# Optimization experiments

Measured on AMD Instinct MI355X. Metric: run time of the kernel, lower is better.

The kernel has to match this reference:

```python
import jax, jax.numpy as jnp
import numpy as np

N = 64       # number of sites / qubits
CHI = 32     # bond dimension chi_max
D = 2        # physical dim (== label dim l)
BATCH = 262144
STD = 0.001  # init noise, matches MPS.initialize_params


def setup_inputs() -> dict:
    key = jax.random.key(0)
    kx, k0, kc, kn = jax.random.split(key, 4)
    # X: [N, batch, d] -- each X[i] contracts with site i's physical leg
    X = jax.random.normal(kx, (N, BATCH, D), dtype=jnp.float32)
    # core0: (d, chi), one-hot column 0 plus noise
    core0 = jnp.zeros((D, CHI), jnp.float32).at[:, 0].set(1.0)
    core0 = core0 + STD * jax.random.normal(k0, (D, CHI), dtype=jnp.float32)
    # middle cores: (N-1, chi, d, chi), identity stacked over d plus noise
    eye = jnp.eye(CHI, dtype=jnp.float32)                      # (chi, chi)
    mid = jnp.broadcast_to(eye[:, None, :], (CHI, D, CHI))     # (chi, d, chi)
    cores = jnp.broadcast_to(mid, (N - 1, CHI, D, CHI))
    cores = cores + STD * jax.random.normal(kc, (N - 1, CHI, D, CHI), dtype=jnp.float32)
    # coreN: (chi, d), one-hot row 0 plus noise
    coreN = jnp.zeros((CHI, D), jnp.float32).at[0].set(1.0)
    coreN = coreN + STD * jax.random.normal(kn, (CHI, D), dtype=jnp.float32)
    return {"X": X, "core0": core0, "cores": cores, "coreN": coreN}


def reference(X, core0, cores, coreN):
    # Sequential MPS chain contraction:
    #   v <- X[0] @ core0                       (batch, chi)
    #   v <- einsum('ab,bqc,aq->ac', v, core_i, X[i])   for i = 1..N-1
    #   out = |v @ coreN|                       (batch, l)
    v0 = jnp.einsum('aq,qc->ac', X[0], core0)  # (B, chi)

    def step(v, inp):
        x, core = inp  # x: (B, d), core: (chi, d, chi)
        # contract bond then physical leg, keeping only (B, chi) resident
        v_new = jnp.einsum('ab,bqc,aq->ac', v, core, x)
        return v_new, None

    v, _ = jax.lax.scan(step, v0, (X[1:], cores))
    out = jnp.einsum('ac,cq->aq', v, coreN)    # (B, l)
    return jnp.abs(out)
```

## Files before the change

### kernel.cpp

```cpp
#include <hip/hip_runtime.h>
#include <hip/hip_bf16.h>

#define BATCH 262144
#define NSITES 64
#define NJ 2
#define BLOCK_BATCH (64 * NJ)

typedef __attribute__((ext_vector_type(8))) short short8;
typedef __attribute__((ext_vector_type(4))) float f32x4;

__device__ __forceinline__ unsigned cvt_pk_bf16(float a, float b) {
  unsigned r;
  asm("v_cvt_pk_bf16_f32 %0, %1, %2" : "=v"(r) : "v"(a), "v"(b));
  return r;
}

__device__ __forceinline__ int qmap(int k) {
  return (((k >> 2) & 1) << 4) | (((k >> 3) & 3) << 2) | (k & 3);
}

__global__ void pack_E(const float* __restrict__ cores, unsigned short* __restrict__ Ep) {
  int idx = blockIdx.x * 256 + threadIdx.x;
  if (idx >= (NSITES - 1) * 2048) return;
  int t = idx & 7;
  int l = (idx >> 3) & 63;
  int f = (idx >> 9) & 3;
  int p = idx >> 11;
  int g = l >> 4, col = l & 15;
  int m = f >> 1, h = f & 1;
  int k = 8 * g + t, c = h * 16 + col;
  int b = qmap(k);
  float val = cores[((p * 32 + b) * 2 + m) * 32 + c] - ((b == c) ? 1.0f : 0.0f);
  __hip_bfloat16 hv = __float2bfloat16(val);
  Ep[idx] = *(unsigned short*)&hv;
}

__device__ __forceinline__ void gll16(const void* g, void* l) {
  __builtin_amdgcn_global_load_lds(
      (const __attribute__((address_space(1))) unsigned*)g,
      (__attribute__((address_space(3))) unsigned*)l, 16, 0, 0);
}

#define BODYJ(jj, xx0, xx1)                                                     \
  {                                                                             \
    union { short8 s8; unsigned u[4]; } vb;                                     \
    vb.u[0] = cvt_pk_bf16(v[jj][0], v[jj][1]);                                  \
    vb.u[1] = cvt_pk_bf16(v[jj][2], v[jj][3]);                                  \
    vb.u[2] = cvt_pk_bf16(v[jj][4], v[jj][5]);                                  \
    vb.u[3] = cvt_pk_bf16(v[jj][6], v[jj][7]);                                  \
    const f32x4 z = {0.f, 0.f, 0.f, 0.f};                                       \
    f32x4 r0lo = __builtin_amdgcn_mfma_f32_16x16x32_bf16(A0, vb.s8, z, 0, 0, 0); \
    f32x4 r0hi = __builtin_amdgcn_mfma_f32_16x16x32_bf16(A1, vb.s8, z, 0, 0, 0); \
    f32x4 r1lo = __builtin_amdgcn_mfma_f32_16x16x32_bf16(A2, vb.s8, z, 0, 0, 0); \
    f32x4 r1hi = __builtin_amdgcn_mfma_f32_16x16x32_bf16(A3, vb.s8, z, 0, 0, 0); \
    const float ss = (xx0) + (xx1);                                             \
    _Pragma("unroll") for (int t = 0; t < 4; ++t) {                             \
      v[jj][t] = ss * v[jj][t] + (xx0)*r0lo[t] + (xx1)*r1lo[t];                 \
      v[jj][4 + t] = ss * v[jj][4 + t] + (xx0)*r0hi[t] + (xx1)*r1hi[t];         \
    }                                                                           \
  }

__global__ __launch_bounds__(256, 8) void mps_chain_kernel(
    const float* __restrict__ X, const float* __restrict__ core0,
    const float* __restrict__ coreN, const unsigned short* __restrict__ Ep,
    float* __restrict__ out) {
  __shared__ __align__(16) char Elds[2][4096];
  const int tid = threadIdx.x;
  const int lane = tid & 63;
  const int wave = tid >> 6;
  const int col = lane & 15;
  const int g = lane >> 4;
  const int abase = blockIdx.x * BLOCK_BATCH + wave * (16 * NJ);
  const char* Epc = (const char*)Ep;

  gll16(Epc + (size_t)tid * 16, &Elds[0][wave * 1024]);

  float c0[2][8];
#pragma unroll
  for (int m = 0; m < 2; ++m)
#pragma unroll
    for (int t = 0; t < 8; ++t) c0[m][t] = core0[m * 32 + qmap(8 * g + t)];

  float v[NJ][8];
#pragma unroll
  for (int jj = 0; jj < NJ; ++jj) {
    const float2 xj = *(const float2*)(X + 2 * (size_t)(abase + jj * 16 + col));
#pragma unroll
    for (int t = 0; t < 8; ++t) v[jj][t] = xj.x * c0[0][t] + xj.y * c0[1][t];
  }

  float xl[NJ], xh[NJ];
#pragma unroll
  for (int jj = 0; jj < NJ; ++jj) {
    const float2 t_ =
        *(const float2*)(X + 2 * ((size_t)1 * BATCH + abase + jj * 16 + col));
    xl[jj] = t_.x;
    xh[jj] = t_.y;
  }
  __syncthreads();

#pragma unroll 1
  for (int s = 1; s < NSITES; ++s) {
    const int buf = (s - 1) & 1;
    if (s < NSITES - 1)
      gll16(Epc + (size_t)s * 4096 + (size_t)tid * 16, &Elds[buf ^ 1][wave * 1024]);

    const size_t sx = (s + 1 < NSITES) ? (size_t)(s + 1) : (size_t)(NSITES - 1);
    float2 xn[NJ];
#pragma unroll
    for (int jj = 0; jj < NJ; ++jj)
      xn[jj] = *(const float2*)(X + 2 * (sx * BATCH + abase + jj * 16 + col));

    const short8* ep = (const short8*)&Elds[buf][lane * 16];
    const short8 A0 = ep[0], A1 = ep[64], A2 = ep[128], A3 = ep[192];

    BODYJ(0, xl[0], xh[0]);
    BODYJ(1, xl[1], xh[1]);

#pragma unroll
    for (int jj = 0; jj < NJ; ++jj) {
      xl[jj] = xn[jj].x;
      xh[jj] = xn[jj].y;
    }
    __syncthreads();
  }

  float cN[8][2];
#pragma unroll
  for (int t = 0; t < 8; ++t) {
    cN[t][0] = coreN[qmap(8 * g + t) * 2 + 0];
    cN[t][1] = coreN[qmap(8 * g + t) * 2 + 1];
  }
#pragma unroll
  for (int jj = 0; jj < NJ; ++jj) {
    float p0 = 0.f, p1 = 0.f;
#pragma unroll
    for (int t = 0; t < 8; ++t) {
      p0 += v[jj][t] * cN[t][0];
      p1 += v[jj][t] * cN[t][1];
    }
    p0 += __shfl_xor(p0, 16);
    p0 += __shfl_xor(p0, 32);
    p1 += __shfl_xor(p1, 16);
    p1 += __shfl_xor(p1, 32);
    if (g == 0) {
      const int a = abase + jj * 16 + col;
      out[2 * a] = fabsf(p0);
      out[2 * a + 1] = fabsf(p1);
    }
  }
}

extern "C" void kernel_launch(void* const* d_in, const int* in_sizes, int n_in,
                              void* d_out, int out_size, void* d_ws, size_t ws_size,
                              hipStream_t stream) {
  const float* X = (const float*)d_in[0];
  const float* core0 = (const float*)d_in[1];
  const float* cores = (const float*)d_in[2];
  const float* coreN = (const float*)d_in[3];
  float* out = (float*)d_out;
  unsigned short* Ep = (unsigned short*)d_ws;

  hipLaunchKernelGGL(pack_E, dim3(((NSITES - 1) * 2048 + 255) / 256), dim3(256), 0, stream,
                     cores, Ep);
  hipLaunchKernelGGL(mps_chain_kernel, dim3(BATCH / BLOCK_BATCH), dim3(256), 0, stream, X,
                     core0, coreN, Ep, out);
}
```

Baseline: 115.7 us.

## Stage four sites of cores per barrier and process four batch tiles per wave

The middle-core matrices are now staged into LDS four sites at a time, double-buffered, so there is one barrier per four chain steps instead of one per step. Each wave now handles four 16-row batch tiles instead of two, reusing the same loaded A fragments for more MFMAs. The explicit one-step-ahead prefetch of X is removed; X is loaded inside each step, which relies on the compiler's unrolling to hide the latency. LDS use per block grows to 32 KB and the occupancy hint drops from 8 to 4 blocks, trading thread-level parallelism for more instruction-level parallelism.

```diff
diff --git a/kernel.cpp b/kernel.cpp
--- a/kernel.cpp
+++ b/kernel.cpp
@@ -3,8 +3,9 @@
 
 #define BATCH 262144
 #define NSITES 64
-#define NJ 2
-#define BLOCK_BATCH (64 * NJ)
+#define NJ 4
+#define BLOCK_BATCH 256
+#define SS 4
 
 typedef __attribute__((ext_vector_type(8))) short short8;
 typedef __attribute__((ext_vector_type(4))) float f32x4;
@@ -41,30 +42,36 @@
       (__attribute__((address_space(3))) unsigned*)l, 16, 0, 0);
 }
 
-#define BODYJ(jj, xx0, xx1)                                                     \
+#define STEPK(bufp, k_, s_)                                                     \
   {                                                                             \
-    union { short8 s8; unsigned u[4]; } vb;                                     \
-    vb.u[0] = cvt_pk_bf16(v[jj][0], v[jj][1]);                                  \
-    vb.u[1] = cvt_pk_bf16(v[jj][2], v[jj][3]);                                  \
-    vb.u[2] = cvt_pk_bf16(v[jj][4], v[jj][5]);                                  \
-    vb.u[3] = cvt_pk_bf16(v[jj][6], v[jj][7]);                                  \
-    const f32x4 z = {0.f, 0.f, 0.f, 0.f};                                       \
-    f32x4 r0lo = __builtin_amdgcn_mfma_f32_16x16x32_bf16(A0, vb.s8, z, 0, 0, 0); \
-    f32x4 r0hi = __builtin_amdgcn_mfma_f32_16x16x32_bf16(A1, vb.s8, z, 0, 0, 0); \
-    f32x4 r1lo = __builtin_amdgcn_mfma_f32_16x16x32_bf16(A2, vb.s8, z, 0, 0, 0); \
-    f32x4 r1hi = __builtin_amdgcn_mfma_f32_16x16x32_bf16(A3, vb.s8, z, 0, 0, 0); \
-    const float ss = (xx0) + (xx1);                                             \
-    _Pragma("unroll") for (int t = 0; t < 4; ++t) {                             \
-      v[jj][t] = ss * v[jj][t] + (xx0)*r0lo[t] + (xx1)*r1lo[t];                 \
-      v[jj][4 + t] = ss * v[jj][4 + t] + (xx0)*r0hi[t] + (xx1)*r1hi[t];         \
+    const short8* ep = (const short8*)&Elds[bufp][(k_)*4096 + lane * 16];       \
+    const short8 A0 = ep[0], A1 = ep[64], A2 = ep[128], A3 = ep[192];           \
+    _Pragma("unroll") for (int jj = 0; jj < NJ; ++jj) {                         \
+      const float2 xj =                                                         \
+          *(const float2*)(Xl + 2 * ((size_t)(s_)*BATCH + jj * 16));            \
+      union { short8 s8; unsigned u[4]; } vb;                                   \
+      vb.u[0] = cvt_pk_bf16(v[jj][0], v[jj][1]);                                \
+      vb.u[1] = cvt_pk_bf16(v[jj][2], v[jj][3]);                                \
+      vb.u[2] = cvt_pk_bf16(v[jj][4], v[jj][5]);                                \
+      vb.u[3] = cvt_pk_bf16(v[jj][6], v[jj][7]);                                \
+      const f32x4 z = {0.f, 0.f, 0.f, 0.f};                                     \
+      f32x4 r0lo = __builtin_amdgcn_mfma_f32_16x16x32_bf16(A0, vb.s8, z, 0, 0, 0); \
+      f32x4 r0hi = __builtin_amdgcn_mfma_f32_16x16x32_bf16(A1, vb.s8, z, 0, 0, 0); \
+      f32x4 r1lo = __builtin_amdgcn_mfma_f32_16x16x32_bf16(A2, vb.s8, z, 0, 0, 0); \
+      f32x4 r1hi = __builtin_amdgcn_mfma_f32_16x16x32_bf16(A3, vb.s8, z, 0, 0, 0); \
+      const float x0s = xj.x, x1s = xj.y, sss = x0s + x1s;                      \
+      _Pragma("unroll") for (int t = 0; t < 4; ++t) {                           \
+        v[jj][t] = sss * v[jj][t] + x0s * r0lo[t] + x1s * r1lo[t];              \
+        v[jj][4 + t] = sss * v[jj][4 + t] + x0s * r0hi[t] + x1s * r1hi[t];      \
+      }                                                                         \
     }                                                                           \
   }
 
-__global__ __launch_bounds__(256, 8) void mps_chain_kernel(
+__global__ __launch_bounds__(256, 4) void mps_chain_kernel(
     const float* __restrict__ X, const float* __restrict__ core0,
     const float* __restrict__ coreN, const unsigned short* __restrict__ Ep,
     float* __restrict__ out) {
-  __shared__ __align__(16) char Elds[2][4096];
+  __shared__ __align__(16) char Elds[2][SS * 4096];
   const int tid = threadIdx.x;
   const int lane = tid & 63;
   const int wave = tid >> 6;
@@ -72,8 +79,12 @@
   const int g = lane >> 4;
   const int abase = blockIdx.x * BLOCK_BATCH + wave * (16 * NJ);
   const char* Epc = (const char*)Ep;
+  const float* Xl = X + 2 * (size_t)(abase + col);
 
-  gll16(Epc + (size_t)tid * 16, &Elds[0][wave * 1024]);
+#pragma unroll
+  for (int k = 0; k < SS; ++k)
+    gll16(Epc + (size_t)k * 4096 + (size_t)tid * 16,
+          &Elds[0][k * 4096 + wave * 1024]);
 
   float c0[2][8];
 #pragma unroll
@@ -84,46 +95,33 @@
   float v[NJ][8];
 #pragma unroll
   for (int jj = 0; jj < NJ; ++jj) {
-    const float2 xj = *(const float2*)(X + 2 * (size_t)(abase + jj * 16 + col));
+    const float2 xj = *(const float2*)(Xl + 2 * (size_t)(jj * 16));
 #pragma unroll
     for (int t = 0; t < 8; ++t) v[jj][t] = xj.x * c0[0][t] + xj.y * c0[1][t];
-  }
-
-  float xl[NJ], xh[NJ];
-#pragma unroll
-  for (int jj = 0; jj < NJ; ++jj) {
-    const float2 t_ =
-        *(const float2*)(X + 2 * ((size_t)1 * BATCH + abase + jj * 16 + col));
-    xl[jj] = t_.x;
-    xh[jj] = t_.y;
   }
   __syncthreads();
 
 #pragma unroll 1
-  for (int s = 1; s < NSITES; ++s) {
-    const int buf = (s - 1) & 1;
-    if (s < NSITES - 1)
-      gll16(Epc + (size_t)s * 4096 + (size_t)tid * 16, &Elds[buf ^ 1][wave * 1024]);
+  for (int b = 0; b < 15; ++b) {
+    const int buf = b & 1;
+    const int pn = 4 * (b + 1);
+#pragma unroll
+    for (int k = 0; k < SS; ++k)
+      if (pn + k < NSITES - 1)
+        gll16(Epc + (size_t)(pn + k) * 4096 + (size_t)tid * 16,
+              &Elds[buf ^ 1][k * 4096 + wave * 1024]);
 
-    const size_t sx = (s + 1 < NSITES) ? (size_t)(s + 1) : (size_t)(NSITES - 1);
-    float2 xn[NJ];
-#pragma unroll
-    for (int jj = 0; jj < NJ; ++jj)
-      xn[jj] = *(const float2*)(X + 2 * (sx * BATCH + abase + jj * 16 + col));
-
-    const short8* ep = (const short8*)&Elds[buf][lane * 16];
-    const short8 A0 = ep[0], A1 = ep[64], A2 = ep[128], A3 = ep[192];
-
-    BODYJ(0, xl[0], xh[0]);
-    BODYJ(1, xl[1], xh[1]);
-
-#pragma unroll
-    for (int jj = 0; jj < NJ; ++jj) {
-      xl[jj] = xn[jj].x;
-      xh[jj] = xn[jj].y;
-    }
+    const int s0 = 1 + 4 * b;
+    STEPK(buf, 0, s0 + 0);
+    STEPK(buf, 1, s0 + 1);
+    STEPK(buf, 2, s0 + 2);
+    STEPK(buf, 3, s0 + 3);
     __syncthreads();
   }
+
+  STEPK(1, 0, 61);
+  STEPK(1, 1, 62);
+  STEPK(1, 2, 63);
 
   float cN[8][2];
 #pragma unroll
```

Result: slower. 127.1 us (+9.8%).

## Load core fragments directly from global, drop LDS staging and barriers, NJ=4

Applied to the files above, without the earlier changes.

Removes the LDS double-buffer and per-site __syncthreads; each wave now reads its bf16 core fragments straight from global memory (L1/L2-resident) and loads X for the current site without software prefetch. Each wave also handles four 16-sample groups instead of two, which raises MFMA work per core-fragment load and lowers occupancy (launch bounds 4). The trade-off is exposed global-load latency each step, since X and core loads are no longer prefetched, in exchange for removing the barriers and LDS traffic.

```diff
diff --git a/kernel.cpp b/kernel.cpp
--- a/kernel.cpp
+++ b/kernel.cpp
@@ -3,8 +3,8 @@
 
 #define BATCH 262144
 #define NSITES 64
-#define NJ 2
-#define BLOCK_BATCH (64 * NJ)
+#define NJ 4
+#define BLOCK_BATCH 256
 
 typedef __attribute__((ext_vector_type(8))) short short8;
 typedef __attribute__((ext_vector_type(4))) float f32x4;
@@ -35,12 +35,6 @@
   Ep[idx] = *(unsigned short*)&hv;
 }
 
-__device__ __forceinline__ void gll16(const void* g, void* l) {
-  __builtin_amdgcn_global_load_lds(
-      (const __attribute__((address_space(1))) unsigned*)g,
-      (__attribute__((address_space(3))) unsigned*)l, 16, 0, 0);
-}
-
 #define BODYJ(jj, xx0, xx1)                                                     \
   {                                                                             \
     union { short8 s8; unsigned u[4]; } vb;                                     \
@@ -60,20 +54,16 @@
     }                                                                           \
   }
 
-__global__ __launch_bounds__(256, 8) void mps_chain_kernel(
+__global__ __launch_bounds__(256, 4) void mps_chain_kernel(
     const float* __restrict__ X, const float* __restrict__ core0,
     const float* __restrict__ coreN, const unsigned short* __restrict__ Ep,
     float* __restrict__ out) {
-  __shared__ __align__(16) char Elds[2][4096];
   const int tid = threadIdx.x;
   const int lane = tid & 63;
   const int wave = tid >> 6;
   const int col = lane & 15;
   const int g = lane >> 4;
   const int abase = blockIdx.x * BLOCK_BATCH + wave * (16 * NJ);
-  const char* Epc = (const char*)Ep;
-
-  gll16(Epc + (size_t)tid * 16, &Elds[0][wave * 1024]);
 
   float c0[2][8];
 #pragma unroll
@@ -89,40 +79,26 @@
     for (int t = 0; t < 8; ++t) v[jj][t] = xj.x * c0[0][t] + xj.y * c0[1][t];
   }
 
-  float xl[NJ], xh[NJ];
-#pragma unroll
-  for (int jj = 0; jj < NJ; ++jj) {
-    const float2 t_ =
-        *(const float2*)(X + 2 * ((size_t)1 * BATCH + abase + jj * 16 + col));
-    xl[jj] = t_.x;
-    xh[jj] = t_.y;
-  }
-  __syncthreads();
+  const char* ep_base = (const char*)Ep + (size_t)lane * 16;
+  const float* xs = X + 2 * ((size_t)BATCH + abase + col);
 
 #pragma unroll 1
   for (int s = 1; s < NSITES; ++s) {
-    const int buf = (s - 1) & 1;
-    if (s < NSITES - 1)
-      gll16(Epc + (size_t)s * 4096 + (size_t)tid * 16, &Elds[buf ^ 1][wave * 1024]);
+    const short8* ep = (const short8*)ep_base;
+    const short8 A0 = ep[0], A1 = ep[64], A2 = ep[128], A3 = ep[192];
 
-    const size_t sx = (s + 1 < NSITES) ? (size_t)(s + 1) : (size_t)(NSITES - 1);
-    float2 xn[NJ];
+    float2 xj[NJ];
 #pragma unroll
     for (int jj = 0; jj < NJ; ++jj)
-      xn[jj] = *(const float2*)(X + 2 * (sx * BATCH + abase + jj * 16 + col));
+      xj[jj] = *(const float2*)(xs + 2 * (jj * 16));
 
-    const short8* ep = (const short8*)&Elds[buf][lane * 16];
-    const short8 A0 = ep[0], A1 = ep[64], A2 = ep[128], A3 = ep[192];
+    BODYJ(0, xj[0].x, xj[0].y);
+    BODYJ(1, xj[1].x, xj[1].y);
+    BODYJ(2, xj[2].x, xj[2].y);
+    BODYJ(3, xj[3].x, xj[3].y);
 
-    BODYJ(0, xl[0], xh[0]);
-    BODYJ(1, xl[1], xh[1]);
-
-#pragma unroll
-    for (int jj = 0; jj < NJ; ++jj) {
-      xl[jj] = xn[jj].x;
-      xh[jj] = xn[jj].y;
-    }
-    __syncthreads();
+    ep_base += 4096;
+    xs += 2 * (size_t)BATCH;
   }
 
   float cN[8][2];
```

New measurement: 104.6 us. -9.6%, faster.
